# Optimization experiments

Hardware: AMD Instinct MI355X
Metric: run time of the kernel (lower is better)

Reference implementation:

```python
import jax, jax.numpy as jnp
import numpy as np

N = 2048        # tokens (batch*seq)
H = 4096        # hidden_size (LLaMA-7B)
I = 11008       # intermediate_size (LLaMA-7B)
QMAX = 127.0    # int8 symmetric quant range


def setup_inputs() -> dict:
    key = jax.random.key(0)
    ks = jax.random.split(key, 6)
    # pre-quantized int8 activations (stored as int32) + per-token dynamic scales
    x_q = jax.random.randint(ks[0], (N, H), -127, 128, dtype=jnp.int32)
    x_scale = jax.random.uniform(ks[1], (N,), dtype=jnp.float32) * 0.01 + 1e-4
    # fused [gate; up] int8 weight [2I, H] with per-output-channel scales
    w_gateup = jax.random.randint(ks[2], (2 * I, H), -127, 128, dtype=jnp.int32)
    w_gateup_scale = jax.random.uniform(ks[3], (2 * I,), dtype=jnp.float32) * 0.005 + 1e-4
    # down_proj int8 weight [H, I] with per-output-channel scales
    w_down = jax.random.randint(ks[4], (H, I), -127, 128, dtype=jnp.int32)
    w_down_scale = jax.random.uniform(ks[5], (H,), dtype=jnp.float32) * 0.005 + 1e-4
    return {"x_q": x_q, "x_scale": x_scale, "w_gateup": w_gateup,
            "w_gateup_scale": w_gateup_scale, "w_down": w_down,
            "w_down_scale": w_down_scale}


def reference(x_q, x_scale, w_gateup, w_gateup_scale, w_down, w_down_scale):
    acc = jnp.matmul(x_q, w_gateup.T)                      # [N, 2I] int32
    gateup = acc.astype(jnp.float32) * x_scale[:, None] * w_gateup_scale[None, :]
    # --- fused silu_and_mul + dynamic per-token requantization ---
    gate, up = jnp.split(gateup, 2, axis=-1)               # each [N, I]
    act = jax.nn.silu(gate) * up                           # [N, I]
    s2 = jnp.max(jnp.abs(act), axis=-1) / QMAX             # [N] dynamic scale
    q2 = jnp.clip(jnp.round(act / s2[:, None]), -QMAX, QMAX)  # requantized int8 (as f32)
    out = jnp.matmul(q2, w_down.T.astype(jnp.float32)) * s2[:, None] * w_down_scale[None, :]
    return out                                             # [N, H]
```

## Files before the change

### kernel.cpp

```cpp
#include <hip/hip_runtime.h>
#include <stdint.h>

typedef int i32x4 __attribute__((ext_vector_type(4)));
typedef unsigned short u16x8 __attribute__((ext_vector_type(8)));

#define N_TOK 2048
#define HID   4096
#define INTER 11008
#define TWOI  22016
#define KS1   64
#define KS2   172

#define GLD16(gp, lp) __builtin_amdgcn_global_load_lds( \
    (const __attribute__((address_space(1))) void*)(gp), \
    (__attribute__((address_space(3))) void*)(lp), 16, 0, 0)
#define BAR() __builtin_amdgcn_s_barrier()
#define WVM(n) asm volatile("s_waitcnt vmcnt(" #n ")" ::: "memory")
#define LGKM0() do { asm volatile("s_waitcnt lgkmcnt(0)" ::: "memory"); \
                     __builtin_amdgcn_sched_barrier(0); } while (0)

__device__ __forceinline__ unsigned short f2bf(float f) {
  uint32_t u = __float_as_uint(f);
  uint32_t r = (u + 0x7fffu + ((u >> 16) & 1u)) >> 16;
  return (unsigned short)r;
}

__global__ __launch_bounds__(256) void pack_panel(
    const int* __restrict__ src, uint8_t* __restrict__ dst, int R, int K)
{
  const int u = blockIdx.x * 256 + threadIdx.x;
  const int upk = R * 4;
  const int t = u / upk;
  const int rem = u - t * upk;
  const int r = rem >> 2;
  const int c0 = ((rem & 3) ^ (r & 3)) << 4;
  const int* s = src + (size_t)r * K + t * 64 + c0;
  i32x4 o;
#pragma unroll
  for (int q = 0; q < 4; ++q) {
    i32x4 w = *reinterpret_cast<const i32x4*>(s + q * 4);
    o[q] = (w[0] & 255) | ((w[1] & 255) << 8) | ((w[2] & 255) << 16)
         | ((w[3] & 255) << 24);
  }
  *reinterpret_cast<i32x4*>(dst + (size_t)u * 16) = o;
}

__global__ __launch_bounds__(1024) void zero_mx(float* __restrict__ mx) {
  const int i = blockIdx.x * 1024 + threadIdx.x;
  if (i < N_TOK) mx[i] = 0.0f;
}

__global__ __launch_bounds__(512, 2) void gemm1_k(
    const uint8_t* __restrict__ x8p, const uint8_t* __restrict__ wgp,
    const float* __restrict__ xs, const float* __restrict__ wgs,
    unsigned short* __restrict__ act, float* __restrict__ mx)
{
  __shared__ uint8_t sm[131072];
  const int tid = threadIdx.x;
  const int lane = tid & 63, wid = tid >> 6;
  const int wgm = wid >> 2, wgn = wid & 3;
  const int r15 = lane & 15;
  const int slotC = (((lane >> 4) ^ (r15 & 3)) << 4);

  const int bid = blockIdx.x;
  const int v = (bid & 7) * 86 + (bid >> 3);
  const int mt = v & 7;
  const int nt = v >> 3;

  const uint8_t* pA  = x8p + (size_t)mt * 256 * 64 + tid * 16;
  const uint8_t* pBg = wgp + (size_t)nt * 128 * 64 + tid * 16;
  const uint8_t* pBu = wgp + ((size_t)INTER + nt * 128) * 64 + tid * 16;

  const int arow = (wgm << 7) + r15;
  const int brow = (wgn << 6) + r15;
  i32x4 acc[8][4] = {};

#define STG1(t, s) do {                                        \
    uint8_t* l = sm + (s) * 32768 + tid * 16;                  \
    const uint8_t* a = pA + (size_t)(t) * 131072;              \
    GLD16(a, l);                                               \
    GLD16(a + 8192, l + 8192);                                 \
    GLD16(pBg + (size_t)(t) * 1409024, l + 16384);             \
    GLD16(pBu + (size_t)(t) * 1409024, l + 24576);             \
  } while (0)

  STG1(0, 0); STG1(1, 1); STG1(2, 2);
  WVM(8); BAR();

  for (int t = 0; t < KS1; ++t) {
    const int rem = KS1 - 1 - t;
    const uint8_t* b = sm + (t & 3) * 32768;
    uint8_t* lnx = sm + ((t + 3) & 3) * 32768 + tid * 16;
    i32x4 bv[4], av[4];
#pragma unroll
    for (int n = 0; n < 4; ++n)
      bv[n] = *reinterpret_cast<const i32x4*>(
          b + 16384 + (brow + n * 16) * 64 + slotC);
#pragma unroll
    for (int m = 0; m < 4; ++m)
      av[m] = *reinterpret_cast<const i32x4*>(b + (arow + m * 16) * 64 + slotC);
    if (rem >= 3) {
      GLD16(pBg + (size_t)(t + 3) * 1409024, lnx + 16384);
      GLD16(pBu + (size_t)(t + 3) * 1409024, lnx + 24576);
    }
    BAR();
    LGKM0();
    __builtin_amdgcn_s_setprio(1);
#pragma unroll
    for (int m = 0; m < 4; ++m)
#pragma unroll
      for (int n = 0; n < 4; ++n)
        acc[m][n] = __builtin_amdgcn_mfma_i32_16x16x64_i8(
            av[m], bv[n], acc[m][n], 0, 0, 0);
    __builtin_amdgcn_s_setprio(0);
#pragma unroll
    for (int m = 0; m < 4; ++m)
      av[m] = *reinterpret_cast<const i32x4*>(
          b + (arow + (m + 4) * 16) * 64 + slotC);
    if (rem >= 3) {
      const uint8_t* a = pA + (size_t)(t + 3) * 131072;
      GLD16(a, lnx);
      GLD16(a + 8192, lnx + 8192);
      WVM(8);
    } else if (rem == 2) { WVM(4); }
    else if (rem == 1)   { WVM(0); }
    BAR();
    LGKM0();
    __builtin_amdgcn_s_setprio(1);
#pragma unroll
    for (int m = 0; m < 4; ++m)
#pragma unroll
      for (int n = 0; n < 4; ++n)
        acc[m + 4][n] = __builtin_amdgcn_mfma_i32_16x16x64_i8(
            av[m], bv[n], acc[m + 4][n], 0, 0, 0);
    __builtin_amdgcn_s_setprio(0);
  }
#undef STG1

  __syncthreads();
  float* gs = (float*)sm;
  const int rq = (lane >> 4) << 2;
  if (wgn < 2) {
#pragma unroll
    for (int m = 0; m < 8; ++m) {
#pragma unroll
      for (int n = 0; n < 4; ++n) {
        const int coll = (wgn << 6) + n * 16 + r15;
        const float wsc = wgs[nt * 128 + coll];
#pragma unroll
        for (int r = 0; r < 4; ++r) {
          const int rowl = (wgm << 7) + m * 16 + rq + r;
          const float g = (float)acc[m][n][r] * xs[mt * 256 + rowl] * wsc;
          gs[rowl * 128 + (coll ^ (((rowl >> 2) & 1) << 4))] = g;
        }
      }
    }
  }
  __syncthreads();
  if (wgn >= 2) {
#pragma unroll
    for (int m = 0; m < 8; ++m) {
      float am[4] = {0.f, 0.f, 0.f, 0.f};
#pragma unroll
      for (int n = 0; n < 4; ++n) {
        const int cu = ((wgn - 2) << 6) + n * 16 + r15;
        const float wsc = wgs[INTER + nt * 128 + cu];
#pragma unroll
        for (int r = 0; r < 4; ++r) {
          const int rowl = (wgm << 7) + m * 16 + rq + r;
          const int grow = mt * 256 + rowl;
          const float uv = (float)acc[m][n][r] * xs[grow] * wsc;
          const float g = gs[rowl * 128 + (cu ^ (((rowl >> 2) & 1) << 4))];
          const float a = g / (1.f + __expf(-g)) * uv;
          act[(size_t)grow * INTER + nt * 128 + cu] = f2bf(a);
          am[r] = fmaxf(am[r], __builtin_fabsf(a));
        }
      }
#pragma unroll
      for (int r = 0; r < 4; ++r) {
#pragma unroll
        for (int off = 1; off < 16; off <<= 1)
          am[r] = fmaxf(am[r], __shfl_xor(am[r], off, 64));
      }
      if (r15 == 0) {
#pragma unroll
        for (int r = 0; r < 4; ++r)
          atomicMax((int*)&mx[mt * 256 + (wgm << 7) + m * 16 + rq + r],
                    __float_as_int(am[r]));
      }
    }
  }
}

__global__ __launch_bounds__(256) void quant_k(
    const unsigned short* __restrict__ act, const float* __restrict__ mx,
    uint8_t* __restrict__ q2p)
{
  const int u = blockIdx.x * 256 + threadIdx.x;
  const int t = u >> 13;
  const int rem = u & 8191;
  const int r = rem >> 2;
  const int c0 = ((rem & 3) ^ (r & 3)) << 4;
  const unsigned short* ap = act + (size_t)r * INTER + t * 64 + c0;
  const float inv = 127.0f / fmaxf(mx[r], 1e-30f);
  u16x8 a0 = *reinterpret_cast<const u16x8*>(ap);
  u16x8 a1 = *reinterpret_cast<const u16x8*>(ap + 8);
  i32x4 o;
#pragma unroll
  for (int q = 0; q < 4; ++q) {
    uint32_t d = 0;
#pragma unroll
    for (int b = 0; b < 4; ++b) {
      const int j = q * 4 + b;
      uint32_t aB = (j < 8) ? a0[j] : a1[j - 8];
      float af = __uint_as_float(aB << 16);
      float rr = rintf(af * inv);
      rr = fminf(fmaxf(rr, -127.f), 127.f);
      d |= ((uint32_t)((int)rr & 255)) << (8 * b);
    }
    o[q] = (int)d;
  }
  *reinterpret_cast<i32x4*>(q2p + (size_t)u * 16) = o;
}

__global__ __launch_bounds__(512, 2) void gemm2_k(
    const uint8_t* __restrict__ q2p, const uint8_t* __restrict__ wdp,
    const float* __restrict__ mx, const float* __restrict__ wds,
    float* __restrict__ out)
{
  __shared__ uint8_t sm[98304];
  const int tid = threadIdx.x;
  const int lane = tid & 63, wid = tid >> 6;
  const int wgm = wid >> 2, wgn = wid & 3;
  const int r15 = lane & 15;
  const int slotC = (((lane >> 4) ^ (r15 & 3)) << 4);

  const int bid = blockIdx.x;
  const int v = (bid & 7) * 32 + (bid >> 3);
  const int nt = v >> 4, mt = v & 15;

  const uint8_t* pA = q2p + (size_t)mt * 128 * 64 + tid * 16;
  const uint8_t* pB = wdp + (size_t)nt * 256 * 64 + tid * 16;

  const int arow = (wgm << 6) + r15;
  const int brow = (wgn << 6) + r15;
  i32x4 acc[4][4] = {};

#define STG2(t, s) do {                                        \
    uint8_t* l = sm + (s) * 24576 + tid * 16;                  \
    GLD16(pA + (size_t)(t) * 131072, l);                       \
    const uint8_t* bb = pB + (size_t)(t) * 262144;             \
    GLD16(bb, l + 8192);                                       \
    GLD16(bb + 8192, l + 16384);                               \
  } while (0)

  STG2(0, 0); STG2(1, 1); STG2(2, 2);
  WVM(6); BAR();

  for (int t = 0; t < KS2; ++t) {
    const int rem = KS2 - 1 - t;
    const uint8_t* b = sm + (t & 3) * 24576;
    uint8_t* lnx = sm + ((t + 3) & 3) * 24576 + tid * 16;
    i32x4 bv[4], av[2];
#pragma unroll
    for (int n = 0; n < 4; ++n)
      bv[n] = *reinterpret_cast<const i32x4*>(
          b + 8192 + (brow + n * 16) * 64 + slotC);
#pragma unroll
    for (int m = 0; m < 2; ++m)
      av[m] = *reinterpret_cast<const i32x4*>(b + (arow + m * 16) * 64 + slotC);
    if (rem >= 3) {
      const uint8_t* bb = pB + (size_t)(t + 3) * 262144;
      GLD16(bb, lnx + 8192);
      GLD16(bb + 8192, lnx + 16384);
    }
    BAR();
    LGKM0();
    __builtin_amdgcn_s_setprio(1);
#pragma unroll
    for (int m = 0; m < 2; ++m)
#pragma unroll
      for (int n = 0; n < 4; ++n)
        acc[m][n] = __builtin_amdgcn_mfma_i32_16x16x64_i8(
            av[m], bv[n], acc[m][n], 0, 0, 0);
    __builtin_amdgcn_s_setprio(0);
#pragma unroll
    for (int m = 0; m < 2; ++m)
      av[m] = *reinterpret_cast<const i32x4*>(
          b + (arow + (m + 2) * 16) * 64 + slotC);
    if (rem >= 3) {
      GLD16(pA + (size_t)(t + 3) * 131072, lnx);
      WVM(6);
    } else if (rem == 2) { WVM(3); }
    else if (rem == 1)   { WVM(0); }
    BAR();
    LGKM0();
    __builtin_amdgcn_s_setprio(1);
#pragma unroll
    for (int m = 0; m < 2; ++m)
#pragma unroll
      for (int n = 0; n < 4; ++n)
        acc[m + 2][n] = __builtin_amdgcn_mfma_i32_16x16x64_i8(
            av[m], bv[n], acc[m + 2][n], 0, 0, 0);
    __builtin_amdgcn_s_setprio(0);
  }
#undef STG2

  const int rq = (lane >> 4) << 2;
#pragma unroll
  for (int m = 0; m < 4; ++m) {
#pragma unroll
    for (int r = 0; r < 4; ++r) {
      const int rowl = (wgm << 6) + m * 16 + rq + r;
      const int grow = mt * 128 + rowl;
      const float s2 = mx[grow] * (1.0f / 127.0f);
      float* op = out + (size_t)grow * HID + nt * 256 + (wgn << 6) + r15;
      const float* wp = wds + nt * 256 + (wgn << 6) + r15;
#pragma unroll
      for (int n = 0; n < 4; ++n)
        op[n * 16] = (float)acc[m][n][r] * s2 * wp[n * 16];
    }
  }
}

extern "C" void kernel_launch(void* const* d_in, const int* in_sizes, int n_in,
                              void* d_out, int out_size, void* d_ws, size_t ws_size,
                              hipStream_t stream)
{
  const int*   x_q = (const int*)d_in[0];
  const float* xs  = (const float*)d_in[1];
  const int*   wg  = (const int*)d_in[2];
  const float* wgs = (const float*)d_in[3];
  const int*   wd  = (const int*)d_in[4];
  const float* wds = (const float*)d_in[5];
  float* out = (float*)d_out;

  uint8_t* ws = (uint8_t*)d_ws;
  uint8_t* x8p = ws;
  uint8_t* wgp = x8p + 8388608;
  uint8_t* wdp = wgp + 90177536;
  unsigned short* act = (unsigned short*)(wdp + 45088768);
  float* mx = (float*)((uint8_t*)act + 45088768);
  uint8_t* q2p = (uint8_t*)mx + 8192;

  zero_mx<<<2, 1024, 0, stream>>>(mx);
  pack_panel<<<2048, 256, 0, stream>>>(x_q, x8p, N_TOK, HID);
  pack_panel<<<22016, 256, 0, stream>>>(wg, wgp, TWOI, HID);
  pack_panel<<<11008, 256, 0, stream>>>(wd, wdp, HID, INTER);

  gemm1_k<<<688, 512, 0, stream>>>(x8p, wgp, xs, wgs, act, mx);
  quant_k<<<5504, 256, 0, stream>>>(act, mx, q2p);
  gemm2_k<<<256, 512, 0, stream>>>(q2p, wdp, mx, wds, out);
}
```

Measured before the change: 477.8 us.

## Repack panels per-thread by row, shrink gemm1 tile to 128x128 with smaller LDS

The pack and quant kernels now have each thread handle 256 contiguous source columns of one row and emit four 64-byte chunks, instead of one 16-byte chunk per thread. This makes the source reads more sequential at the cost of much smaller grids (128/1376/688/344 blocks). gemm1 switches from a 256x128 M tile with 128KB LDS to a 128x128 tile with 96KB LDS and 1376 blocks. The goal is better occupancy and load balance, traded against more A/B refetch traffic.

```diff
diff --git a/kernel.cpp b/kernel.cpp
--- a/kernel.cpp
+++ b/kernel.cpp
@@ -25,24 +25,32 @@
   return (unsigned short)r;
 }
 
-__global__ __launch_bounds__(256) void pack_panel(
-    const int* __restrict__ src, uint8_t* __restrict__ dst, int R, int K)
+__global__ __launch_bounds__(256) void pack_panel2(
+    const int* __restrict__ src, uint8_t* __restrict__ dst, int R, int K,
+    int tpr)
 {
   const int u = blockIdx.x * 256 + threadIdx.x;
-  const int upk = R * 4;
-  const int t = u / upk;
-  const int rem = u - t * upk;
-  const int r = rem >> 2;
-  const int c0 = ((rem & 3) ^ (r & 3)) << 4;
-  const int* s = src + (size_t)r * K + t * 64 + c0;
-  i32x4 o;
-#pragma unroll
-  for (int q = 0; q < 4; ++q) {
-    i32x4 w = *reinterpret_cast<const i32x4*>(s + q * 4);
-    o[q] = (w[0] & 255) | ((w[1] & 255) << 8) | ((w[2] & 255) << 16)
-         | ((w[3] & 255) << 24);
-  }
-  *reinterpret_cast<i32x4*>(dst + (size_t)u * 16) = o;
+  const int r = u / tpr;
+  const int j = u - r * tpr;
+  const int perm = r & 3;
+  const int* s = src + (size_t)r * K + j * 256;
+#pragma unroll
+  for (int c = 0; c < 4; ++c) {
+    const int t = j * 4 + c;
+    uint8_t* d = dst + ((size_t)t * R + r) * 64;
+#pragma unroll
+    for (int qs = 0; qs < 4; ++qs) {
+      const int* sp = s + c * 64 + ((qs ^ perm) << 4);
+      i32x4 o;
+#pragma unroll
+      for (int q = 0; q < 4; ++q) {
+        i32x4 w = *reinterpret_cast<const i32x4*>(sp + q * 4);
+        o[q] = (w[0] & 255) | ((w[1] & 255) << 8) | ((w[2] & 255) << 16)
+             | ((w[3] & 255) << 24);
+      }
+      *reinterpret_cast<i32x4*>(d + qs * 16) = o;
+    }
+  }
 }
 
 __global__ __launch_bounds__(1024) void zero_mx(float* __restrict__ mx) {
@@ -54,179 +62,6 @@
     const uint8_t* __restrict__ x8p, const uint8_t* __restrict__ wgp,
     const float* __restrict__ xs, const float* __restrict__ wgs,
     unsigned short* __restrict__ act, float* __restrict__ mx)
-{
-  __shared__ uint8_t sm[131072];
-  const int tid = threadIdx.x;
-  const int lane = tid & 63, wid = tid >> 6;
-  const int wgm = wid >> 2, wgn = wid & 3;
-  const int r15 = lane & 15;
-  const int slotC = (((lane >> 4) ^ (r15 & 3)) << 4);
-
-  const int bid = blockIdx.x;
-  const int v = (bid & 7) * 86 + (bid >> 3);
-  const int mt = v & 7;
-  const int nt = v >> 3;
-
-  const uint8_t* pA  = x8p + (size_t)mt * 256 * 64 + tid * 16;
-  const uint8_t* pBg = wgp + (size_t)nt * 128 * 64 + tid * 16;
-  const uint8_t* pBu = wgp + ((size_t)INTER + nt * 128) * 64 + tid * 16;
-
-  const int arow = (wgm << 7) + r15;
-  const int brow = (wgn << 6) + r15;
-  i32x4 acc[8][4] = {};
-
-#define STG1(t, s) do {                                        \
-    uint8_t* l = sm + (s) * 32768 + tid * 16;                  \
-    const uint8_t* a = pA + (size_t)(t) * 131072;              \
-    GLD16(a, l);                                               \
-    GLD16(a + 8192, l + 8192);                                 \
-    GLD16(pBg + (size_t)(t) * 1409024, l + 16384);             \
-    GLD16(pBu + (size_t)(t) * 1409024, l + 24576);             \
-  } while (0)
-
-  STG1(0, 0); STG1(1, 1); STG1(2, 2);
-  WVM(8); BAR();
-
-  for (int t = 0; t < KS1; ++t) {
-    const int rem = KS1 - 1 - t;
-    const uint8_t* b = sm + (t & 3) * 32768;
-    uint8_t* lnx = sm + ((t + 3) & 3) * 32768 + tid * 16;
-    i32x4 bv[4], av[4];
-#pragma unroll
-    for (int n = 0; n < 4; ++n)
-      bv[n] = *reinterpret_cast<const i32x4*>(
-          b + 16384 + (brow + n * 16) * 64 + slotC);
-#pragma unroll
-    for (int m = 0; m < 4; ++m)
-      av[m] = *reinterpret_cast<const i32x4*>(b + (arow + m * 16) * 64 + slotC);
-    if (rem >= 3) {
-      GLD16(pBg + (size_t)(t + 3) * 1409024, lnx + 16384);
-      GLD16(pBu + (size_t)(t + 3) * 1409024, lnx + 24576);
-    }
-    BAR();
-    LGKM0();
-    __builtin_amdgcn_s_setprio(1);
-#pragma unroll
-    for (int m = 0; m < 4; ++m)
-#pragma unroll
-      for (int n = 0; n < 4; ++n)
-        acc[m][n] = __builtin_amdgcn_mfma_i32_16x16x64_i8(
-            av[m], bv[n], acc[m][n], 0, 0, 0);
-    __builtin_amdgcn_s_setprio(0);
-#pragma unroll
-    for (int m = 0; m < 4; ++m)
-      av[m] = *reinterpret_cast<const i32x4*>(
-          b + (arow + (m + 4) * 16) * 64 + slotC);
-    if (rem >= 3) {
-      const uint8_t* a = pA + (size_t)(t + 3) * 131072;
-      GLD16(a, lnx);
-      GLD16(a + 8192, lnx + 8192);
-      WVM(8);
-    } else if (rem == 2) { WVM(4); }
-    else if (rem == 1)   { WVM(0); }
-    BAR();
-    LGKM0();
-    __builtin_amdgcn_s_setprio(1);
-#pragma unroll
-    for (int m = 0; m < 4; ++m)
-#pragma unroll
-      for (int n = 0; n < 4; ++n)
-        acc[m + 4][n] = __builtin_amdgcn_mfma_i32_16x16x64_i8(
-            av[m], bv[n], acc[m + 4][n], 0, 0, 0);
-    __builtin_amdgcn_s_setprio(0);
-  }
-#undef STG1
-
-  __syncthreads();
-  float* gs = (float*)sm;
-  const int rq = (lane >> 4) << 2;
-  if (wgn < 2) {
-#pragma unroll
-    for (int m = 0; m < 8; ++m) {
-#pragma unroll
-      for (int n = 0; n < 4; ++n) {
-        const int coll = (wgn << 6) + n * 16 + r15;
-        const float wsc = wgs[nt * 128 + coll];
-#pragma unroll
-        for (int r = 0; r < 4; ++r) {
-          const int rowl = (wgm << 7) + m * 16 + rq + r;
-          const float g = (float)acc[m][n][r] * xs[mt * 256 + rowl] * wsc;
-          gs[rowl * 128 + (coll ^ (((rowl >> 2) & 1) << 4))] = g;
-        }
-      }
-    }
-  }
-  __syncthreads();
-  if (wgn >= 2) {
-#pragma unroll
-    for (int m = 0; m < 8; ++m) {
-      float am[4] = {0.f, 0.f, 0.f, 0.f};
-#pragma unroll
-      for (int n = 0; n < 4; ++n) {
-        const int cu = ((wgn - 2) << 6) + n * 16 + r15;
-        const float wsc = wgs[INTER + nt * 128 + cu];
-#pragma unroll
-        for (int r = 0; r < 4; ++r) {
-          const int rowl = (wgm << 7) + m * 16 + rq + r;
-          const int grow = mt * 256 + rowl;
-          const float uv = (float)acc[m][n][r] * xs[grow] * wsc;
-          const float g = gs[rowl * 128 + (cu ^ (((rowl >> 2) & 1) << 4))];
-          const float a = g / (1.f + __expf(-g)) * uv;
-          act[(size_t)grow * INTER + nt * 128 + cu] = f2bf(a);
-          am[r] = fmaxf(am[r], __builtin_fabsf(a));
-        }
-      }
-#pragma unroll
-      for (int r = 0; r < 4; ++r) {
-#pragma unroll
-        for (int off = 1; off < 16; off <<= 1)
-          am[r] = fmaxf(am[r], __shfl_xor(am[r], off, 64));
-      }
-      if (r15 == 0) {
-#pragma unroll
-        for (int r = 0; r < 4; ++r)
-          atomicMax((int*)&mx[mt * 256 + (wgm << 7) + m * 16 + rq + r],
-                    __float_as_int(am[r]));
-      }
-    }
-  }
-}
-
-__global__ __launch_bounds__(256) void quant_k(
-    const unsigned short* __restrict__ act, const float* __restrict__ mx,
-    uint8_t* __restrict__ q2p)
-{
-  const int u = blockIdx.x * 256 + threadIdx.x;
-  const int t = u >> 13;
-  const int rem = u & 8191;
-  const int r = rem >> 2;
-  const int c0 = ((rem & 3) ^ (r & 3)) << 4;
-  const unsigned short* ap = act + (size_t)r * INTER + t * 64 + c0;
-  const float inv = 127.0f / fmaxf(mx[r], 1e-30f);
-  u16x8 a0 = *reinterpret_cast<const u16x8*>(ap);
-  u16x8 a1 = *reinterpret_cast<const u16x8*>(ap + 8);
-  i32x4 o;
-#pragma unroll
-  for (int q = 0; q < 4; ++q) {
-    uint32_t d = 0;
-#pragma unroll
-    for (int b = 0; b < 4; ++b) {
-      const int j = q * 4 + b;
-      uint32_t aB = (j < 8) ? a0[j] : a1[j - 8];
-      float af = __uint_as_float(aB << 16);
-      float rr = rintf(af * inv);
-      rr = fminf(fmaxf(rr, -127.f), 127.f);
-      d |= ((uint32_t)((int)rr & 255)) << (8 * b);
-    }
-    o[q] = (int)d;
-  }
-  *reinterpret_cast<i32x4*>(q2p + (size_t)u * 16) = o;
-}
-
-__global__ __launch_bounds__(512, 2) void gemm2_k(
-    const uint8_t* __restrict__ q2p, const uint8_t* __restrict__ wdp,
-    const float* __restrict__ mx, const float* __restrict__ wds,
-    float* __restrict__ out)
 {
   __shared__ uint8_t sm[98304];
   const int tid = threadIdx.x;
@@ -236,29 +71,30 @@
   const int slotC = (((lane >> 4) ^ (r15 & 3)) << 4);
 
   const int bid = blockIdx.x;
-  const int v = (bid & 7) * 32 + (bid >> 3);
-  const int nt = v >> 4, mt = v & 15;
-
-  const uint8_t* pA = q2p + (size_t)mt * 128 * 64 + tid * 16;
-  const uint8_t* pB = wdp + (size_t)nt * 256 * 64 + tid * 16;
+  const int v = (bid & 7) * 172 + (bid >> 3);
+  const int mt = v & 15;
+  const int nt = v >> 4;
+
+  const uint8_t* pA  = x8p + (size_t)mt * 128 * 64 + tid * 16;
+  const uint8_t* pBg = wgp + (size_t)nt * 128 * 64 + tid * 16;
+  const uint8_t* pBu = wgp + ((size_t)INTER + nt * 128) * 64 + tid * 16;
 
   const int arow = (wgm << 6) + r15;
   const int brow = (wgn << 6) + r15;
   i32x4 acc[4][4] = {};
 
-#define STG2(t, s) do {                                        \
+#define STG1(t, s) do {                                        \
     uint8_t* l = sm + (s) * 24576 + tid * 16;                  \
     GLD16(pA + (size_t)(t) * 131072, l);                       \
-    const uint8_t* bb = pB + (size_t)(t) * 262144;             \
-    GLD16(bb, l + 8192);                                       \
-    GLD16(bb + 8192, l + 16384);                               \
+    GLD16(pBg + (size_t)(t) * 1409024, l + 8192);              \
+    GLD16(pBu + (size_t)(t) * 1409024, l + 16384);             \
   } while (0)
 
-  STG2(0, 0); STG2(1, 1); STG2(2, 2);
+  STG1(0, 0); STG1(1, 1); STG1(2, 2);
   WVM(6); BAR();
 
-  for (int t = 0; t < KS2; ++t) {
-    const int rem = KS2 - 1 - t;
+  for (int t = 0; t < KS1; ++t) {
+    const int rem = KS1 - 1 - t;
     const uint8_t* b = sm + (t & 3) * 24576;
     uint8_t* lnx = sm + ((t + 3) & 3) * 24576 + tid * 16;
     i32x4 bv[4], av[2];
@@ -270,9 +106,8 @@
     for (int m = 0; m < 2; ++m)
       av[m] = *reinterpret_cast<const i32x4*>(b + (arow + m * 16) * 64 + slotC);
     if (rem >= 3) {
-      const uint8_t* bb = pB + (size_t)(t + 3) * 262144;
-      GLD16(bb, lnx + 8192);
-      GLD16(bb + 8192, lnx + 16384);
+      GLD16(pBg + (size_t)(t + 3) * 1409024, lnx + 8192);
+      GLD16(pBu + (size_t)(t + 3) * 1409024, lnx + 16384);
     }
     BAR();
     LGKM0();
@@ -304,6 +139,183 @@
             av[m], bv[n], acc[m + 2][n], 0, 0, 0);
     __builtin_amdgcn_s_setprio(0);
   }
+#undef STG1
+
+  __syncthreads();
+  float* gs = (float*)sm;
+  const int rq = (lane >> 4) << 2;
+  if (wgn < 2) {
+#pragma unroll
+    for (int m = 0; m < 4; ++m) {
+#pragma unroll
+      for (int n = 0; n < 4; ++n) {
+        const int coll = (wgn << 6) + n * 16 + r15;
+        const float wsc = wgs[nt * 128 + coll];
+#pragma unroll
+        for (int r = 0; r < 4; ++r) {
+          const int rowl = (wgm << 6) + m * 16 + rq + r;
+          const float g = (float)acc[m][n][r] * xs[mt * 128 + rowl] * wsc;
+          gs[rowl * 128 + (coll ^ (((rowl >> 2) & 1) << 4))] = g;
+        }
+      }
+    }
+  }
+  __syncthreads();
+  if (wgn >= 2) {
+#pragma unroll
+    for (int m = 0; m < 4; ++m) {
+      float am[4] = {0.f, 0.f, 0.f, 0.f};
+#pragma unroll
+      for (int n = 0; n < 4; ++n) {
+        const int cu = ((wgn - 2) << 6) + n * 16 + r15;
+        const float wsc = wgs[INTER + nt * 128 + cu];
+#pragma unroll
+        for (int r = 0; r < 4; ++r) {
+          const int rowl = (wgm << 6) + m * 16 + rq + r;
+          const int grow = mt * 128 + rowl;
+          const float uv = (float)acc[m][n][r] * xs[grow] * wsc;
+          const float g = gs[rowl * 128 + (cu ^ (((rowl >> 2) & 1) << 4))];
+          const float a = g / (1.f + __expf(-g)) * uv;
+          act[(size_t)grow * INTER + nt * 128 + cu] = f2bf(a);
+          am[r] = fmaxf(am[r], __builtin_fabsf(a));
+        }
+      }
+#pragma unroll
+      for (int r = 0; r < 4; ++r) {
+#pragma unroll
+        for (int off = 1; off < 16; off <<= 1)
+          am[r] = fmaxf(am[r], __shfl_xor(am[r], off, 64));
+      }
+      if (r15 == 0) {
+#pragma unroll
+        for (int r = 0; r < 4; ++r)
+          atomicMax((int*)&mx[mt * 128 + (wgm << 6) + m * 16 + rq + r],
+                    __float_as_int(am[r]));
+      }
+    }
+  }
+}
+
+__global__ __launch_bounds__(256) void quant_k(
+    const unsigned short* __restrict__ act, const float* __restrict__ mx,
+    uint8_t* __restrict__ q2p)
+{
+  const int u = blockIdx.x * 256 + threadIdx.x;
+  const int r = u / 43;
+  const int j = u - r * 43;
+  const int perm = r & 3;
+  const float inv = 127.0f / fmaxf(mx[r], 1e-30f);
+  const unsigned short* ap = act + (size_t)r * INTER + j * 256;
+#pragma unroll
+  for (int c = 0; c < 4; ++c) {
+    const int t = j * 4 + c;
+    uint8_t* d = q2p + ((size_t)t * N_TOK + r) * 64;
+#pragma unroll
+    for (int qs = 0; qs < 4; ++qs) {
+      const unsigned short* sp = ap + c * 64 + ((qs ^ perm) << 4);
+      u16x8 a0 = *reinterpret_cast<const u16x8*>(sp);
+      u16x8 a1 = *reinterpret_cast<const u16x8*>(sp + 8);
+      i32x4 o;
+#pragma unroll
+      for (int q = 0; q < 4; ++q) {
+        uint32_t dd = 0;
+#pragma unroll
+        for (int b = 0; b < 4; ++b) {
+          const int idx = q * 4 + b;
+          uint32_t aB = (idx < 8) ? a0[idx] : a1[idx - 8];
+          float af = __uint_as_float(aB << 16);
+          float rr = rintf(af * inv);
+          rr = fminf(fmaxf(rr, -127.f), 127.f);
+          dd |= ((uint32_t)((int)rr & 255)) << (8 * b);
+        }
+        o[q] = (int)dd;
+      }
+      *reinterpret_cast<i32x4*>(d + qs * 16) = o;
+    }
+  }
+}
+
+__global__ __launch_bounds__(512, 2) void gemm2_k(
+    const uint8_t* __restrict__ q2p, const uint8_t* __restrict__ wdp,
+    const float* __restrict__ mx, const float* __restrict__ wds,
+    float* __restrict__ out)
+{
+  __shared__ uint8_t sm[98304];
+  const int tid = threadIdx.x;
+  const int lane = tid & 63, wid = tid >> 6;
+  const int wgm = wid >> 2, wgn = wid & 3;
+  const int r15 = lane & 15;
+  const int slotC = (((lane >> 4) ^ (r15 & 3)) << 4);
+
+  const int bid = blockIdx.x;
+  const int v = (bid & 7) * 32 + (bid >> 3);
+  const int nt = v >> 4, mt = v & 15;
+
+  const uint8_t* pA = q2p + (size_t)mt * 128 * 64 + tid * 16;
+  const uint8_t* pB = wdp + (size_t)nt * 256 * 64 + tid * 16;
+
+  const int arow = (wgm << 6) + r15;
+  const int brow = (wgn << 6) + r15;
+  i32x4 acc[4][4] = {};
+
+#define STG2(t, s) do {                                        \
+    uint8_t* l = sm + (s) * 24576 + tid * 16;                  \
+    GLD16(pA + (size_t)(t) * 131072, l);                       \
+    const uint8_t* bb = pB + (size_t)(t) * 262144;             \
+    GLD16(bb, l + 8192);                                       \
+    GLD16(bb + 8192, l + 16384);                               \
+  } while (0)
+
+  STG2(0, 0); STG2(1, 1); STG2(2, 2);
+  WVM(6); BAR();
+
+  for (int t = 0; t < KS2; ++t) {
+    const int rem = KS2 - 1 - t;
+    const uint8_t* b = sm + (t & 3) * 24576;
+    uint8_t* lnx = sm + ((t + 3) & 3) * 24576 + tid * 16;
+    i32x4 bv[4], av[2];
+#pragma unroll
+    for (int n = 0; n < 4; ++n)
+      bv[n] = *reinterpret_cast<const i32x4*>(
+          b + 8192 + (brow + n * 16) * 64 + slotC);
+#pragma unroll
+    for (int m = 0; m < 2; ++m)
+      av[m] = *reinterpret_cast<const i32x4*>(b + (arow + m * 16) * 64 + slotC);
+    if (rem >= 3) {
+      const uint8_t* bb = pB + (size_t)(t + 3) * 262144;
+      GLD16(bb, lnx + 8192);
+      GLD16(bb + 8192, lnx + 16384);
+    }
+    BAR();
+    LGKM0();
+    __builtin_amdgcn_s_setprio(1);
+#pragma unroll
+    for (int m = 0; m < 2; ++m)
+#pragma unroll
+      for (int n = 0; n < 4; ++n)
+        acc[m][n] = __builtin_amdgcn_mfma_i32_16x16x64_i8(
+            av[m], bv[n], acc[m][n], 0, 0, 0);
+    __builtin_amdgcn_s_setprio(0);
+#pragma unroll
+    for (int m = 0; m < 2; ++m)
+      av[m] = *reinterpret_cast<const i32x4*>(
+          b + (arow + (m + 2) * 16) * 64 + slotC);
+    if (rem >= 3) {
+      GLD16(pA + (size_t)(t + 3) * 131072, lnx);
+      WVM(6);
+    } else if (rem == 2) { WVM(3); }
+    else if (rem == 1)   { WVM(0); }
+    BAR();
+    LGKM0();
+    __builtin_amdgcn_s_setprio(1);
+#pragma unroll
+    for (int m = 0; m < 2; ++m)
+#pragma unroll
+      for (int n = 0; n < 4; ++n)
+        acc[m + 2][n] = __builtin_amdgcn_mfma_i32_16x16x64_i8(
+            av[m], bv[n], acc[m + 2][n], 0, 0, 0);
+    __builtin_amdgcn_s_setprio(0);
+  }
 #undef STG2
 
   const int rq = (lane >> 4) << 2;
@@ -344,11 +356,11 @@
   uint8_t* q2p = (uint8_t*)mx + 8192;
 
   zero_mx<<<2, 1024, 0, stream>>>(mx);
-  pack_panel<<<2048, 256, 0, stream>>>(x_q, x8p, N_TOK, HID);
-  pack_panel<<<22016, 256, 0, stream>>>(wg, wgp, TWOI, HID);
-  pack_panel<<<11008, 256, 0, stream>>>(wd, wdp, HID, INTER);
-
-  gemm1_k<<<688, 512, 0, stream>>>(x8p, wgp, xs, wgs, act, mx);
-  quant_k<<<5504, 256, 0, stream>>>(act, mx, q2p);
+  pack_panel2<<<128, 256, 0, stream>>>(x_q, x8p, N_TOK, HID, 16);
+  pack_panel2<<<1376, 256, 0, stream>>>(wg, wgp, TWOI, HID, 16);
+  pack_panel2<<<688, 256, 0, stream>>>(wd, wdp, HID, INTER, 43);
+
+  gemm1_k<<<1376, 512, 0, stream>>>(x8p, wgp, xs, wgs, act, mx);
+  quant_k<<<344, 256, 0, stream>>>(act, mx, q2p);
   gemm2_k<<<256, 512, 0, stream>>>(q2p, wdp, mx, wds, out);
 }
```

Result: slower. 600.9 us (+25.8%).
